# Performance work log

Measured on AMD Instinct MI355X. Metric: run time of the kernel, lower is better.

Reference implementation:

```python
import jax, jax.numpy as jnp
import numpy as np

RES = (512, 512)
MAX_VAL = 100.0
OBJ_WIDTH = 5
N_ITERS = 5
SIGMA = 0.2


def setup_inputs() -> dict:
    key = jax.random.key(0)
    ks = jax.random.split(key, 6)
    H, W = RES
    x = jax.random.uniform(ks[0], (1, H, W, 2), jnp.float32) * 2.0 - 1.0  # query grid in [-1,1]
    boundary_types = jax.random.randint(ks[1], (H, W), 0, 2, jnp.int32)
    boundary_conditions = jax.random.uniform(ks[2], (H, W), jnp.float32)
    B_enc = SIGMA * jax.random.normal(ks[3], (64, 2), jnp.float32)  # GaussianEncoding(0.2, 2, 64)
    Wh = jax.random.normal(ks[4], (4, 128, 128), jnp.float32) / jnp.sqrt(128.0)
    W_out = jax.random.normal(ks[5], (128, 1), jnp.float32) / jnp.sqrt(128.0)
    return {"x": x, "boundary_types": boundary_types,
            "boundary_conditions": boundary_conditions,
            "B_enc": B_enc, "Wh": Wh, "W_out": W_out}


def _box_filter(a, width):
    # width x width mean filter, 'same' padding (F.conv2d with ones/width^2 kernel)
    k = jnp.ones((1, 1, width, width), a.dtype) / float(width * width)
    return jax.lax.conv_general_dilated(a[None, None], k, (1, 1), "SAME")[0, 0]


def _grid_sample_2d(img, grid):
    # img [H,W]; grid [N,2] with (x,y) in [-1,1]; bilinear, align_corners=True, border padding
    H, W = img.shape
    ix = jnp.clip((grid[:, 0] + 1.0) * 0.5 * (W - 1), 0.0, W - 1.0)
    iy = jnp.clip((grid[:, 1] + 1.0) * 0.5 * (H - 1), 0.0, H - 1.0)
    x0 = jnp.floor(ix).astype(jnp.int32)
    y0 = jnp.floor(iy).astype(jnp.int32)
    x1 = jnp.clip(x0 + 1, 0, W - 1)
    y1 = jnp.clip(y0 + 1, 0, H - 1)
    wx = ix - x0
    wy = iy - y0
    return (img[y0, x0] * (1 - wx) * (1 - wy) + img[y0, x1] * wx * (1 - wy)
            + img[y1, x0] * (1 - wx) * wy + img[y1, x1] * wx * wy)


def _solve(V0, C, boundary_types, boundary_conditions):
    # 5 Jacobi-style 8-neighbor stencil passes: free cells take the neighbor
    # average plus local cost; boundary cells are pinned to their conditions.
    free = boundary_types == 0

    def step(V, _):
        Vp = jnp.pad(V, 1, mode="edge")
        nb = (Vp[:-2, :-2] + Vp[:-2, 1:-1] + Vp[:-2, 2:]
              + Vp[1:-1, :-2] + Vp[1:-1, 2:]
              + Vp[2:, :-2] + Vp[2:, 1:-1] + Vp[2:, 2:]) / 8.0
        return jnp.where(free, nb + C, boundary_conditions), None

    V, _ = jax.lax.scan(step, V0, None, length=N_ITERS)
    return V


def reference(x, boundary_types, boundary_conditions, B_enc, Wh, W_out):
    H, W = RES
    free = boundary_types == 0
    # V init: max_val everywhere, boundary cells pinned (obj_inds = boundary_types > 0)
    V0 = jnp.where(free, jnp.float32(MAX_VAL), boundary_conditions)

    # Gaussian random Fourier feature encoding of 0.5 + 0.5*x -> 128 dims
    xq = 0.5 + 0.5 * x.reshape(-1, 2)
    vp = (2.0 * jnp.pi) * (xq @ B_enc.T)            # [N, 64]
    enc = jnp.concatenate([jnp.cos(vp), jnp.sin(vp)], axis=-1)  # [N, 128]

    # FullyFusedMLP: 4 hidden ReLU layers of 128 neurons, linear 1-dim output, no bias
    h = enc
    for i in range(Wh.shape[0]):
        h = jax.nn.relu(h @ Wh[i])
    C = (h @ W_out).reshape(H, W)
    C_pos = jax.nn.relu(C)

    # extra cost: box-filtered obstacle boundary values splashed onto free cells
    obj = boundary_conditions * (boundary_types == 1) * (boundary_conditions > 0)
    extra = _box_filter(obj, OBJ_WIDTH) * free
    Cs = C_pos + extra

    out_grid = _solve(V0, Cs, boundary_types, boundary_conditions)
    out = _grid_sample_2d(out_grid, x.reshape(-1, 2)).reshape(H, W)
    return out, C
```

## Files before the change

kernel.cpp:

```cpp
#include <hip/hip_runtime.h>
#include <hip/hip_bf16.h>


typedef unsigned short ushort_t;
typedef short short8 __attribute__((ext_vector_type(8)));
typedef float floatx16 __attribute__((ext_vector_type(16)));
typedef unsigned int uintx4 __attribute__((ext_vector_type(4)));

#define HH 512
#define WW 512
#define NPIX (HH*WW)

__device__ inline unsigned int pk_bf16(float a, float b) {
    __hip_bfloat162 h = __float22bfloat162_rn(float2{a, b});
    return *(unsigned int*)&h;
}
__device__ inline void async_copy16(void* lds, const void* g) {
    __builtin_amdgcn_global_load_lds(
        (const __attribute__((address_space(1))) unsigned int*)g,
        (__attribute__((address_space(3))) unsigned int*)lds, 16, 0, 0);
}

__global__ __launch_bounds__(256) void prep_kernel(const float* __restrict__ Wh,
                                                   ushort_t* __restrict__ WT) {
    __shared__ float trans[32][129];
    const int t = threadIdx.x;
    const int l = blockIdx.x >> 2, n0 = (blockIdx.x & 3) * 32;
    const int nl = t & 31, k0 = t >> 5;
    #pragma unroll
    for (int pass = 0; pass < 16; ++pass) {
        int k = pass * 8 + k0;
        trans[nl][k] = Wh[l * 16384 + k * 128 + n0 + nl];
    }
    __syncthreads();
    #pragma unroll
    for (int c = 0; c < 2; ++c) {
        int idx = c * 256 + t;
        int nl2 = idx >> 4, P = idx & 15;
        int n = n0 + nl2;
        int cc = P ^ (n & 15);
        int ks = cc >> 1, Hq = cc & 1;
        int base = (ks >> 1) * 32 + (ks & 1) * 16 + Hq * 4;
        unsigned int w0 = pk_bf16(trans[nl2][base + 0],  trans[nl2][base + 1]);
        unsigned int w1 = pk_bf16(trans[nl2][base + 2],  trans[nl2][base + 3]);
        unsigned int w2 = pk_bf16(trans[nl2][base + 8],  trans[nl2][base + 9]);
        unsigned int w3 = pk_bf16(trans[nl2][base + 10], trans[nl2][base + 11]);
        ((uint4*)WT)[(l * 128 + n) * 16 + P] = uint4{w0, w1, w2, w3};
    }
}

__global__ __launch_bounds__(512, 2) void mlp_kernel(const float* __restrict__ x,
                                                     const ushort_t* __restrict__ WT,
                                                     const float* __restrict__ benc,
                                                     const float* __restrict__ wout,
                                                     float* __restrict__ C_ws,
                                                     float* __restrict__ outbuf) {
    __shared__ __align__(16) ushort_t wlds[128 * 128];
    const int tid = threadIdx.x;
    const int lane = tid & 63, wave = tid >> 6;
    const int m = lane & 31, Hh = lane >> 5;
    const int p0 = blockIdx.x * 256 + wave * 32;

    #pragma unroll
    for (int c2 = 0; c2 < 4; ++c2) {
        int base = c2 * 512 + wave * 64;
        async_copy16(&wlds[base * 8], (const char*)WT + (base + lane) * 16);
    }

    uintx4 fragv[8];

    {
        float2 xv = ((const float2*)x)[p0 + m];
        float xq0 = 0.5f + 0.5f * xv.x, xq1 = 0.5f + 0.5f * xv.y;
        #pragma unroll
        for (int ks = 0; ks < 8; ++ks) {
            const int i = ks >> 1, par = ks & 1;
            #pragma unroll
            for (int jp = 0; jp < 4; ++jp) {
                int nu = i * 32 + par * 16 + Hh * 4 + (jp & 1) * 2 + (jp >> 1) * 8;
                int f = nu & 63;
                float4 b = *(const float4*)&benc[2 * f];
                float t0 = __builtin_amdgcn_fractf(xq0 * b.x + xq1 * b.y);
                float t1 = __builtin_amdgcn_fractf(xq0 * b.z + xq1 * b.w);
                float v0, v1;
                if (ks < 4) { v0 = __builtin_amdgcn_cosf(t0); v1 = __builtin_amdgcn_cosf(t1); }
                else        { v0 = __builtin_amdgcn_sinf(t0); v1 = __builtin_amdgcn_sinf(t1); }
                fragv[ks][jp] = pk_bf16(v0, v1);
            }
        }
    }
    __syncthreads();

    floatx16 acc[4];
    #pragma unroll 1
    for (int l = 0; l < 4; ++l) {
        #pragma unroll
        for (int i = 0; i < 4; ++i) acc[i] = (floatx16)(0.0f);

        #pragma unroll
        for (int ks = 0; ks < 8; ++ks) {
            short8 bf = __builtin_bit_cast(short8, fragv[ks]);
            #pragma unroll
            for (int i = 0; i < 4; ++i) {
                int n = i * 32 + m;
                int cc = 2 * ks + Hh;
                short8 av = *(const short8*)&wlds[(n << 7) + ((cc ^ (n & 15)) << 3)];
                acc[i] = __builtin_amdgcn_mfma_f32_32x32x16_bf16(av, bf, acc[i], 0, 0, 0);
            }
        }
        if (l == 3) break;

        __syncthreads();

        #pragma unroll
        for (int c2 = 0; c2 < 4; ++c2) {
            int base = c2 * 512 + wave * 64;
            async_copy16(&wlds[base * 8],
                         (const char*)WT + (l + 1) * 32768 + (base + lane) * 16);
        }

        #pragma unroll
        for (int ks = 0; ks < 8; ++ks) {
            const int i = ks >> 1, par = ks & 1;
            fragv[ks][0] = pk_bf16(fmaxf(acc[i][8 * par + 0], 0.0f),
                                   fmaxf(acc[i][8 * par + 1], 0.0f));
            fragv[ks][1] = pk_bf16(fmaxf(acc[i][8 * par + 2], 0.0f),
                                   fmaxf(acc[i][8 * par + 3], 0.0f));
            fragv[ks][2] = pk_bf16(fmaxf(acc[i][8 * par + 4], 0.0f),
                                   fmaxf(acc[i][8 * par + 5], 0.0f));
            fragv[ks][3] = pk_bf16(fmaxf(acc[i][8 * par + 6], 0.0f),
                                   fmaxf(acc[i][8 * par + 7], 0.0f));
        }

        __syncthreads();
    }

    float s = 0.0f;
    #pragma unroll
    for (int i = 0; i < 4; ++i) {
        #pragma unroll
        for (int rq = 0; rq < 4; ++rq) {
            float4 wv = *(const float4*)&wout[i * 32 + rq * 8 + 4 * Hh];
            s += fmaxf(acc[i][rq * 4 + 0], 0.0f) * wv.x
               + fmaxf(acc[i][rq * 4 + 1], 0.0f) * wv.y
               + fmaxf(acc[i][rq * 4 + 2], 0.0f) * wv.z
               + fmaxf(acc[i][rq * 4 + 3], 0.0f) * wv.w;
        }
    }
    s += __shfl_xor(s, 32);
    if (Hh == 0) {
        C_ws[p0 + m] = s;
        outbuf[NPIX + p0 + m] = s;
    }
}

__global__ __launch_bounds__(256) void fused_solve_kernel(const int* __restrict__ bt,
                                                          const float* __restrict__ bc,
                                                          const float* __restrict__ C_ws,
                                                          float* __restrict__ Vfin) {
    __shared__ float Va[30 * 32];
    __shared__ float Vb[30 * 32];
    __shared__ float Wp[30 * 32];
    const int tid = threadIdx.x;
    const int gx0 = (blockIdx.x & 31) * 16 - 7, gy0 = (blockIdx.x >> 5) * 16 - 7;

    for (int c = tid; c < 30 * 32; c += 256) {
        int li = c >> 5, lj = c & 31;
        int gi = gy0 + li, gj = gx0 + lj;
        float v = 0.0f;
        if (lj < 30 && gi >= 0 && gi < HH && gj >= 0 && gj < WW) {
            int g = gi * WW + gj;
            float b = bc[g];
            if (bt[g] == 1 && b > 0.0f) v = b;
        }
        Va[c] = v;
    }
    __syncthreads();

    for (int c = tid; c < 30 * 32; c += 256) {
        int li = c >> 5, lj = c & 31;
        int gi = gy0 + li, gj = gx0 + lj;
        float w = -1.0f, v0 = 0.0f;
        if (li >= 2 && li < 28 && lj >= 2 && lj < 28 &&
            gi >= 0 && gi < HH && gj >= 0 && gj < WW) {
            int g = gi * WW + gj;
            if (bt[g] == 0) {
                float s = 0.0f;
                #pragma unroll
                for (int di = 0; di < 5; ++di)
                    #pragma unroll
                    for (int dj = 0; dj < 5; ++dj)
                        s += Va[(li + di - 2) * 32 + lj + dj - 2];
                w = fmaxf(C_ws[g], 0.0f) + s * 0.04f;
                v0 = 100.0f;
            } else {
                float b = bc[g];
                w = -b - 1.0f;
                v0 = b;
            }
        }
        Wp[c] = w;
        Vb[c] = v0;
    }
    __syncthreads();

    float* src = Vb;
    float* dst = Va;
    #pragma unroll 1
    for (int t = 0; t < 5; ++t) {
        for (int c = tid; c < 26 * 32; c += 256) {
            int li = 2 + (c >> 5), lj = c & 31;
            if (lj < 2 || lj >= 28) continue;
            float w = Wp[li * 32 + lj];
            float v;
            if (w < 0.0f) {
                v = -w - 1.0f;
            } else {
                int gi = gy0 + li, gj = gx0 + lj;
                int um = (gi > 0)      ? li - 1 : li;
                int dp = (gi < HH - 1) ? li + 1 : li;
                int lm = (gj > 0)      ? lj - 1 : lj;
                int rp = (gj < WW - 1) ? lj + 1 : lj;
                float s = src[um * 32 + lm] + src[um * 32 + lj] + src[um * 32 + rp]
                        + src[li * 32 + lm]                     + src[li * 32 + rp]
                        + src[dp * 32 + lm] + src[dp * 32 + lj] + src[dp * 32 + rp];
                v = s * 0.125f + w;
            }
            dst[li * 32 + lj] = v;
        }
        __syncthreads();
        float* tmp = src; src = dst; dst = tmp;
    }

    {
        int li = 7 + (tid >> 4), lj = 7 + (tid & 15);
        Vfin[(gy0 + li) * WW + gx0 + lj] = src[li * 32 + lj];
    }
}

__global__ void sample_kernel(const float* __restrict__ x,
                              const float* __restrict__ V,
                              float* __restrict__ out) {
    int idx = blockIdx.x * 256 + threadIdx.x;
    float2 g2 = ((const float2*)x)[idx];
    float ix = (g2.x + 1.0f) * 0.5f * 511.0f;
    float iy = (g2.y + 1.0f) * 0.5f * 511.0f;
    ix = fminf(fmaxf(ix, 0.0f), 511.0f);
    iy = fminf(fmaxf(iy, 0.0f), 511.0f);
    int x0 = (int)floorf(ix), y0 = (int)floorf(iy);
    int x1 = min(x0 + 1, 511), y1 = min(y0 + 1, 511);
    float wx = ix - (float)x0, wy = iy - (float)y0;
    float v00 = V[y0 * 512 + x0], v01 = V[y0 * 512 + x1];
    float v10 = V[y1 * 512 + x0], v11 = V[y1 * 512 + x1];
    float v = v00 * (1.0f - wx) * (1.0f - wy) + v01 * wx * (1.0f - wy)
            + v10 * (1.0f - wx) * wy          + v11 * wx * wy;
    out[idx] = v;
}

extern "C" void kernel_launch(void* const* d_in, const int* in_sizes, int n_in,
                              void* d_out, int out_size, void* d_ws, size_t ws_size,
                              hipStream_t stream) {
    const float* x    = (const float*)d_in[0];
    const int*   bt   = (const int*)d_in[1];
    const float* bc   = (const float*)d_in[2];
    const float* benc = (const float*)d_in[3];
    const float* Wh   = (const float*)d_in[4];
    const float* wout = (const float*)d_in[5];

    char* ws = (char*)d_ws;
    ushort_t* WT   = (ushort_t*)(ws + 4096);
    float*    C_ws = (float*)(ws + 262144);
    float*    Vfin = (float*)(ws + 262144 + 3 * (1 << 20));
    float*    outp = (float*)d_out;

    prep_kernel<<<16, 256, 0, stream>>>(Wh, WT);
    mlp_kernel<<<1024, 512, 0, stream>>>(x, WT, benc, wout, C_ws, outp);
    fused_solve_kernel<<<1024, 256, 0, stream>>>(bt, bc, C_ws, Vfin);
    sample_kernel<<<1024, 256, 0, stream>>>(x, Vfin, outp);
}
```

Measured before the change: 120.2 us.

## Double-buffer MLP layer weights in LDS and unroll layer loop

Switches the weight staging to two 32KB LDS buffers so each layer's weights are loaded asynchronously while an earlier layer's MFMAs run. This removes one barrier per layer and the wait between the weight load and the next layer's compute. The layer loop is fully unrolled, and the swizzled LDS offsets are precomputed once per thread. In exchange the block uses twice the LDS (64KB), which could limit occupancy at 2 blocks per CU, and the unrolled code raises register pressure.

```diff
diff --git a/kernel.cpp b/kernel.cpp
--- a/kernel.cpp
+++ b/kernel.cpp
@@ -49,23 +49,67 @@
     }
 }
 
+template<int BUF>
+__device__ __forceinline__ void klayer(const ushort_t* __restrict__ wlds,
+                                       const int (&inn)[8],
+                                       const uintx4 (&fragv)[8],
+                                       floatx16 (&acc)[4]) {
+    #pragma unroll
+    for (int i = 0; i < 4; ++i) acc[i] = (floatx16)(0.0f);
+    #pragma unroll
+    for (int ks = 0; ks < 8; ++ks) {
+        short8 bf = __builtin_bit_cast(short8, fragv[ks]);
+        #pragma unroll
+        for (int i = 0; i < 4; ++i) {
+            short8 av = *(const short8*)((const char*)wlds + BUF * 32768 + i * 8192 + inn[ks]);
+            acc[i] = __builtin_amdgcn_mfma_f32_32x32x16_bf16(av, bf, acc[i], 0, 0, 0);
+        }
+    }
+}
+
+__device__ __forceinline__ void xform_all(uintx4 (&fragv)[8], const floatx16 (&acc)[4]) {
+    #pragma unroll
+    for (int ks = 0; ks < 8; ++ks) {
+        const int i = ks >> 1, par = ks & 1;
+        fragv[ks][0] = pk_bf16(fmaxf(acc[i][8 * par + 0], 0.0f),
+                               fmaxf(acc[i][8 * par + 1], 0.0f));
+        fragv[ks][1] = pk_bf16(fmaxf(acc[i][8 * par + 2], 0.0f),
+                               fmaxf(acc[i][8 * par + 3], 0.0f));
+        fragv[ks][2] = pk_bf16(fmaxf(acc[i][8 * par + 4], 0.0f),
+                               fmaxf(acc[i][8 * par + 5], 0.0f));
+        fragv[ks][3] = pk_bf16(fmaxf(acc[i][8 * par + 6], 0.0f),
+                               fmaxf(acc[i][8 * par + 7], 0.0f));
+    }
+}
+
+__device__ __forceinline__ void stage_layer(ushort_t* wlds, int buf,
+                                            const char* src, int wave, int lane) {
+    #pragma unroll
+    for (int c2 = 0; c2 < 4; ++c2) {
+        int base = c2 * 512 + wave * 64;
+        async_copy16(&wlds[buf * 16384 + base * 8], src + (base + lane) * 16);
+    }
+}
+
 __global__ __launch_bounds__(512, 2) void mlp_kernel(const float* __restrict__ x,
                                                      const ushort_t* __restrict__ WT,
                                                      const float* __restrict__ benc,
                                                      const float* __restrict__ wout,
                                                      float* __restrict__ C_ws,
                                                      float* __restrict__ outbuf) {
-    __shared__ __align__(16) ushort_t wlds[128 * 128];
+    __shared__ __align__(16) ushort_t wlds[2 * 128 * 128];
     const int tid = threadIdx.x;
     const int lane = tid & 63, wave = tid >> 6;
     const int m = lane & 31, Hh = lane >> 5;
     const int p0 = blockIdx.x * 256 + wave * 32;
 
-    #pragma unroll
-    for (int c2 = 0; c2 < 4; ++c2) {
-        int base = c2 * 512 + wave * 64;
-        async_copy16(&wlds[base * 8], (const char*)WT + (base + lane) * 16);
-    }
+    stage_layer(wlds, 0, (const char*)WT, wave, lane);
+    stage_layer(wlds, 1, (const char*)WT + 32768, wave, lane);
+
+    int inn[8];
+    #pragma unroll
+    for (int ks = 0; ks < 8; ++ks)
+        inn[ks] = m * 256 + ((((2 * ks + Hh) ^ (m & 15))) << 4);
 
     uintx4 fragv[8];
 
@@ -92,48 +136,18 @@
     __syncthreads();
 
     floatx16 acc[4];
-    #pragma unroll 1
-    for (int l = 0; l < 4; ++l) {
-        #pragma unroll
-        for (int i = 0; i < 4; ++i) acc[i] = (floatx16)(0.0f);
-
-        #pragma unroll
-        for (int ks = 0; ks < 8; ++ks) {
-            short8 bf = __builtin_bit_cast(short8, fragv[ks]);
-            #pragma unroll
-            for (int i = 0; i < 4; ++i) {
-                int n = i * 32 + m;
-                int cc = 2 * ks + Hh;
-                short8 av = *(const short8*)&wlds[(n << 7) + ((cc ^ (n & 15)) << 3)];
-                acc[i] = __builtin_amdgcn_mfma_f32_32x32x16_bf16(av, bf, acc[i], 0, 0, 0);
-            }
-        }
-        if (l == 3) break;
-
-        __syncthreads();
-
-        #pragma unroll
-        for (int c2 = 0; c2 < 4; ++c2) {
-            int base = c2 * 512 + wave * 64;
-            async_copy16(&wlds[base * 8],
-                         (const char*)WT + (l + 1) * 32768 + (base + lane) * 16);
-        }
-
-        #pragma unroll
-        for (int ks = 0; ks < 8; ++ks) {
-            const int i = ks >> 1, par = ks & 1;
-            fragv[ks][0] = pk_bf16(fmaxf(acc[i][8 * par + 0], 0.0f),
-                                   fmaxf(acc[i][8 * par + 1], 0.0f));
-            fragv[ks][1] = pk_bf16(fmaxf(acc[i][8 * par + 2], 0.0f),
-                                   fmaxf(acc[i][8 * par + 3], 0.0f));
-            fragv[ks][2] = pk_bf16(fmaxf(acc[i][8 * par + 4], 0.0f),
-                                   fmaxf(acc[i][8 * par + 5], 0.0f));
-            fragv[ks][3] = pk_bf16(fmaxf(acc[i][8 * par + 6], 0.0f),
-                                   fmaxf(acc[i][8 * par + 7], 0.0f));
-        }
-
-        __syncthreads();
-    }
+    klayer<0>(wlds, inn, fragv, acc);
+    __syncthreads();
+    stage_layer(wlds, 0, (const char*)WT + 2 * 32768, wave, lane);
+    xform_all(fragv, acc);
+    klayer<1>(wlds, inn, fragv, acc);
+    __syncthreads();
+    stage_layer(wlds, 1, (const char*)WT + 3 * 32768, wave, lane);
+    xform_all(fragv, acc);
+    klayer<0>(wlds, inn, fragv, acc);
+    __syncthreads();
+    xform_all(fragv, acc);
+    klayer<1>(wlds, inn, fragv, acc);
 
     float s = 0.0f;
     #pragma unroll
```

Result: no change. 118.1 us (-1.7%).
